# Kernel tuning notes

Hardware: AMD Instinct MI355X
Metric: run time of the kernel (lower is better)

The kernel has to match this reference:

```python
import jax, jax.numpy as jnp
import numpy as np

T, K_FR, K_D, A = 2000, 400, 400, 100
EPS = 1e-24


def setup_inputs() -> dict:
    key = jax.random.key(0)
    ks = jax.random.split(key, 5)
    t = jnp.arange(T, dtype=jnp.float32)                      # uniform grid, dt = 1
    mask_spikes_fr = jax.random.randint(ks[0], (T, K_FR), 0, 2, dtype=jnp.int32)
    X_fr = jax.random.normal(ks[1], (T, K_FR, A), dtype=jnp.float32)
    theta = jax.random.normal(ks[2], (A,), dtype=jnp.float32) * 0.01  # keep r = exp(u) ~ O(1)
    phi_d = jax.random.normal(ks[3], (K_D,), dtype=jnp.float32)
    phi_fr = jax.random.normal(ks[4], (K_FR,), dtype=jnp.float32)
    return {"t": t, "mask_spikes_fr": mask_spikes_fr, "X_fr": X_fr,
            "theta": theta, "phi_d": phi_d, "phi_fr": phi_fr}


def _forward(t, mask_spikes_fr, X_fr, theta, phi_d, phi_fr, lam_mmd=1.0):
    dt = t[1] - t[0]
    m = mask_spikes_fr.astype(X_fr.dtype)                     # [T, K_fr] spike indicator
    u = jnp.einsum('tka,a->tk', X_fr, theta)                  # membrane potential
    r = jnp.exp(u)                                            # non_linearity = 'exp'
    # per-trial point-process log-likelihood: [K_fr]
    ll = jnp.sum(jnp.log(1.0 - jnp.exp(-dt * r) + EPS) * m - dt * r * (1.0 - m), axis=0)
    # score-function gradient of log-likelihood w.r.t. theta (r detached): [K_fr, A]
    r_d = jax.lax.stop_gradient(r)
    exp_r = jnp.exp(r_d * dt)
    g_ll = dt * jnp.einsum('tka,tk->ka', X_fr, r_d / (exp_r - 1.0 - EPS) * m) \
         - dt * jnp.einsum('tka,tk->ka', X_fr, r_d * (1.0 - m))
    # gramians from per-trial features phi
    g_ff = phi_fr[:, None] * phi_fr[None, :]                  # [K_fr, K_fr], symmetric
    g_df = phi_d[:, None] * phi_fr[None, :]                   # [K_d, K_fr]
    g_dd = phi_d[:, None] * phi_d[None, :]                    # [K_d, K_d], symmetric
    K_fr = phi_fr.shape[0]
    K_d = phi_d.shape[0]
    n_fr = K_fr * (K_fr - 1) // 2                             # number of triu (k=1) pairs
    n_d = K_d * (K_d - 1) // 2
    row_ff = jnp.sum(g_ff, axis=1)
    diag_ff = jnp.diagonal(g_ff)
    # mean over i<j of (ll_i + ll_j) * g_ff[i,j]; g_ff symmetric => (full - diag)/2
    mmd_grad = (jnp.dot(ll, row_ff) - jnp.dot(ll, diag_ff)) / n_fr \
             - 2.0 * jnp.mean(ll[None, :] * g_df)
    # mean over i<j of (g_ll_i + g_ll_j) * g_ff[i,j] per component a, minus cross term
    grad_theta = (jnp.einsum('ij,ia->a', g_ff, g_ll) - jnp.einsum('i,ia->a', diag_ff, g_ll)) / n_fr \
               - 2.0 * jnp.einsum('df,fa->a', g_df, g_ll) / (K_d * K_fr)
    # unbiased MMD: off-diagonal means of gramians
    tri_ff = (jnp.sum(g_ff) - jnp.sum(diag_ff)) / 2.0 / n_fr
    tri_dd = (jnp.sum(g_dd) - jnp.sum(jnp.diagonal(g_dd))) / 2.0 / n_d
    mmd = tri_dd + tri_ff - 2.0 * jnp.mean(g_df)
    return lam_mmd * mmd_grad, lam_mmd * grad_theta, mmd


def reference(t, mask_spikes_fr, X_fr, theta, phi_d, phi_fr):
    return _forward(t, mask_spikes_fr, X_fr, theta, phi_d, phi_fr)
```

## Files before the change

### kernel.cpp

```cpp
#include <hip/hip_runtime.h>

#define T_LEN   2000
#define K_FR    400
#define K_D     400
#define A_DIM   100
#define N_ROWS  (T_LEN * K_FR)
#define RPB     64
#define TILE_F  (RPB * A_DIM)
#define TILE_V4 (TILE_F / 4)
#define NBATCH  (N_ROWS / RPB)
#define EPSF    1e-24f
#define MAIN_BLOCKS 1024


__global__ void mmdglm_setup(const float* __restrict__ phi_d,
                             const float* __restrict__ phi_fr,
                             float* __restrict__ c,
                             float* __restrict__ gth_acc,
                             double* __restrict__ mmdg_acc,
                             float* __restrict__ out)
{
    __shared__ float w1[8], w2[8], w3[8], w4[8];
    __shared__ float sums[4];
    const int tid = threadIdx.x;
    const float vfr = (tid < K_FR) ? phi_fr[tid] : 0.f;
    const float vd  = (tid < K_D)  ? phi_d[tid]  : 0.f;
    float s1 = vfr, s2 = vfr * vfr, s3 = vd, s4 = vd * vd;
    #pragma unroll
    for (int off = 1; off < 64; off <<= 1) {
        s1 += __shfl_xor(s1, off);
        s2 += __shfl_xor(s2, off);
        s3 += __shfl_xor(s3, off);
        s4 += __shfl_xor(s4, off);
    }
    const int wave = tid >> 6, lane = tid & 63;
    if (lane == 0) { w1[wave] = s1; w2[wave] = s2; w3[wave] = s3; w4[wave] = s4; }
    __syncthreads();
    if (tid == 0) {
        float a = 0, b = 0, cc = 0, d = 0;
        for (int i = 0; i < 8; ++i) { a += w1[i]; b += w2[i]; cc += w3[i]; d += w4[i]; }
        sums[0] = a; sums[1] = b; sums[2] = cc; sums[3] = d;
    }
    __syncthreads();
    const float S_fr = sums[0], Q_fr = sums[1], S_d = sums[2], Q_d = sums[3];
    const float n_fr = (float)(K_FR * (K_FR - 1) / 2);
    const float n_d  = (float)(K_D * (K_D - 1) / 2);
    if (tid < K_FR) {
        const float p = phi_fr[tid];
        c[tid] = (S_fr * p - p * p) / n_fr
               - 2.0f * S_d * p / (float)(K_D * K_FR);
    }
    if (tid < A_DIM) gth_acc[tid] = 0.f;
    if (tid == 511) *mmdg_acc = 0.0;
    if (tid == 0) {
        const float mmd = (S_d * S_d - Q_d) / (2.0f * n_d)
                        + (S_fr * S_fr - Q_fr) / (2.0f * n_fr)
                        - 2.0f * S_d * S_fr / (float)(K_D * K_FR);
        out[101] = mmd;
    }
}

__global__ __launch_bounds__(256)
void mmdglm_main(const float* __restrict__ X,
                 const int*   __restrict__ mask,
                 const float* __restrict__ theta,
                 const float* __restrict__ tvec,
                 const float* __restrict__ c,
                 float*  __restrict__ gth_acc,
                 double* __restrict__ mmdg_acc)
{
    __shared__ __align__(16) float tile[TILE_F];
    __shared__ float lred[4];
    const int tid  = threadIdx.x;
    const int slot = tid >> 2;
    const int part = tid & 3;

    float th[25];
    #pragma unroll
    for (int j = 0; j < 25; ++j) th[j] = theta[part * 25 + j];

    const float dt = tvec[1] - tvec[0];

    float acc[25];
    #pragma unroll
    for (int j = 0; j < 25; ++j) acc[j] = 0.f;
    float llacc = 0.f;

    for (int b = blockIdx.x; b < NBATCH; b += gridDim.x) {
        const int row0 = b * RPB;
        const float4* src = (const float4*)(X + (size_t)row0 * A_DIM);
        for (int i = tid; i < TILE_V4; i += 256)
            ((float4*)tile)[i] = src[i];
        __syncthreads();

        const int row = row0 + slot;
        const float* xp = tile + 25 * tid;
        float x[25];
        float u = 0.f;
        #pragma unroll
        for (int j = 0; j < 25; ++j) { x[j] = xp[j]; u = fmaf(x[j], th[j], u); }
        u += __shfl_xor(u, 1);
        u += __shfl_xor(u, 2);

        const float r  = __expf(u);
        const int   m  = mask[row];
        const float ck = c[row - (row / K_FR) * K_FR];
        float w, llt;
        if (m) {
            const float eneg = __expf(-dt * r);
            const float epos = __expf(dt * r);
            llt = __logf(1.0f - eneg + EPSF);
            w   = dt * r / (epos - 1.0f - EPSF);
        } else {
            llt = -dt * r;
            w   = -dt * r;
        }
        const float cw = ck * w;
        if (part == 0) llacc = fmaf(ck, llt, llacc);
        #pragma unroll
        for (int j = 0; j < 25; ++j) acc[j] = fmaf(cw, x[j], acc[j]);
        __syncthreads();
    }

    #pragma unroll
    for (int j = 0; j < 25; ++j) tile[tid * 25 + j] = acc[j];
    __syncthreads();
    if (tid < A_DIM) {
        const int p = tid / 25, j = tid - p * 25;
        float s = 0.f;
        for (int sl = 0; sl < RPB; ++sl)
            s += tile[(sl * 4 + p) * 25 + j];
        atomicAdd(&gth_acc[tid], s);
    }

    float l = llacc;
    #pragma unroll
    for (int off = 1; off < 64; off <<= 1) l += __shfl_xor(l, off);
    const int wave = tid >> 6, lane = tid & 63;
    if (lane == 0) lred[wave] = l;
    __syncthreads();
    if (tid == 0)
        atomicAdd(mmdg_acc, (double)(lred[0] + lred[1] + lred[2] + lred[3]));
}

__global__ void mmdglm_finalize(const double* __restrict__ mmdg_acc,
                                const float* __restrict__ gth_acc,
                                float* __restrict__ out)
{
    const int tid = threadIdx.x;
    if (tid == 0) out[0] = (float)(*mmdg_acc);
    if (tid >= 1 && tid <= 100) out[tid] = gth_acc[tid - 1];
}

extern "C" void kernel_launch(void* const* d_in, const int* in_sizes, int n_in,
                              void* d_out, int out_size, void* d_ws, size_t ws_size,
                              hipStream_t stream) {
    const float* t      = (const float*)d_in[0];
    const int*   mask   = (const int*)  d_in[1];
    const float* X      = (const float*)d_in[2];
    const float* theta  = (const float*)d_in[3];
    const float* phi_d  = (const float*)d_in[4];
    const float* phi_fr = (const float*)d_in[5];
    float* out = (float*)d_out;

    char* ws = (char*)d_ws;
    double* mmdg_acc = (double*)ws;
    float*  gth_acc  = (float*)(ws + 8);
    float*  c        = (float*)(ws + 416);

    mmdglm_setup<<<1, 512, 0, stream>>>(phi_d, phi_fr, c, gth_acc, mmdg_acc, out);
    mmdglm_main<<<MAIN_BLOCKS, 256, 0, stream>>>(X, mask, theta, t, c, gth_acc, mmdg_acc);
    mmdglm_finalize<<<1, 128, 0, stream>>>(mmdg_acc, gth_acc, out);
}
```

Before: 464.1 us.

## Double-buffer X tiles with async global-to-LDS loads

Replaces the synchronous float4 copy of each 64-row X tile into shared memory with `global_load_lds` DMA-style loads into a double buffer. The next tile is prefetched while the current one is computed, and one barrier per iteration is dropped. The aim is to hide global memory latency in a kernel that streams X far below peak bandwidth. The cost is doubled LDS per block, which may lower occupancy. Correctness also depends on the barrier waiting for outstanding LDS-direct loads.

Measured after the change: 458.2 us. Within noise of the previous version (-1.3%).

```diff
diff --git a/kernel.cpp b/kernel.cpp
--- a/kernel.cpp
+++ b/kernel.cpp
@@ -7,7 +7,6 @@
 #define N_ROWS  (T_LEN * K_FR)
 #define RPB     64
 #define TILE_F  (RPB * A_DIM)
-#define TILE_V4 (TILE_F / 4)
 #define NBATCH  (N_ROWS / RPB)
 #define EPSF    1e-24f
 #define MAIN_BLOCKS 1024
@@ -60,6 +59,18 @@
     }
 }
 
+__device__ __forceinline__ void stage_tile(const float* __restrict__ g0,
+                                           float* l0, int wave, int lane)
+{
+    for (int c = wave; c < 25; c += 4) {
+        const float* g = g0 + (c << 8) + (lane << 2);
+        float* l = l0 + (c << 8);
+        __builtin_amdgcn_global_load_lds(
+            (const __attribute__((address_space(1))) void*)g,
+            (__attribute__((address_space(3))) void*)l, 16, 0, 0);
+    }
+}
+
 __global__ __launch_bounds__(256)
 void mmdglm_main(const float* __restrict__ X,
                  const int*   __restrict__ mask,
@@ -69,9 +80,10 @@
                  float*  __restrict__ gth_acc,
                  double* __restrict__ mmdg_acc)
 {
-    __shared__ __align__(16) float tile[TILE_F];
+    __shared__ __align__(16) float buf[2][TILE_F];
     __shared__ float lred[4];
     const int tid  = threadIdx.x;
+    const int wave = tid >> 6, lane = tid & 63;
     const int slot = tid >> 2;
     const int part = tid & 3;
 
@@ -86,15 +98,19 @@
     for (int j = 0; j < 25; ++j) acc[j] = 0.f;
     float llacc = 0.f;
 
-    for (int b = blockIdx.x; b < NBATCH; b += gridDim.x) {
-        const int row0 = b * RPB;
-        const float4* src = (const float4*)(X + (size_t)row0 * A_DIM);
-        for (int i = tid; i < TILE_V4; i += 256)
-            ((float4*)tile)[i] = src[i];
+    int t = blockIdx.x;
+    stage_tile(X + (size_t)t * TILE_F, buf[0], wave, lane);
+    int cur = 0;
+
+    for (; t < NBATCH; t += gridDim.x) {
         __syncthreads();
 
-        const int row = row0 + slot;
-        const float* xp = tile + 25 * tid;
+        const int tn = t + (int)gridDim.x;
+        if (tn < NBATCH)
+            stage_tile(X + (size_t)tn * TILE_F, buf[cur ^ 1], wave, lane);
+
+        const int row = t * RPB + slot;
+        const float* xp = buf[cur] + 25 * tid;
         float x[25];
         float u = 0.f;
         #pragma unroll
@@ -119,24 +135,26 @@
         if (part == 0) llacc = fmaf(ck, llt, llacc);
         #pragma unroll
         for (int j = 0; j < 25; ++j) acc[j] = fmaf(cw, x[j], acc[j]);
-        __syncthreads();
+
+        cur ^= 1;
     }
+    __syncthreads();
 
+    float* red = &buf[0][0];
     #pragma unroll
-    for (int j = 0; j < 25; ++j) tile[tid * 25 + j] = acc[j];
+    for (int j = 0; j < 25; ++j) red[tid * 25 + j] = acc[j];
     __syncthreads();
     if (tid < A_DIM) {
         const int p = tid / 25, j = tid - p * 25;
         float s = 0.f;
         for (int sl = 0; sl < RPB; ++sl)
-            s += tile[(sl * 4 + p) * 25 + j];
+            s += red[(sl * 4 + p) * 25 + j];
         atomicAdd(&gth_acc[tid], s);
     }
 
     float l = llacc;
     #pragma unroll
     for (int off = 1; off < 64; off <<= 1) l += __shfl_xor(l, off);
-    const int wave = tid >> 6, lane = tid & 63;
     if (lane == 0) lred[wave] = l;
     __syncthreads();
     if (tid == 0)
```
